# Performance work log

Measured on AMD Instinct MI355X. Metric: run time of the kernel, lower is better.

## Reference

```python
import jax, jax.numpy as jnp
import numpy as np

DIM_MODEL = 512
INV_SCALE = DIM_MODEL ** (-0.5)  # NOTE: source DIVIDES by this, i.e. multiplies scores by sqrt(d)


def setup_inputs() -> dict:
    key = jax.random.key(0)
    ks = jax.random.split(key, 9)
    B, LQ, LKV, D = 32, 64, 4096, DIM_MODEL
    lim = 1.0 / np.sqrt(D)  # torch Linear default init range
    return {
        "x1": jax.random.normal(ks[0], (B, LQ, D), dtype=jnp.float32),
        "x2": jax.random.normal(ks[1], (B, LKV, D), dtype=jnp.float32),
        "mask": jnp.zeros((B, LQ, LKV), dtype=bool),
        "wq": jax.random.uniform(ks[2], (D, D), jnp.float32, -lim, lim),
        "bq": jax.random.uniform(ks[3], (D,), jnp.float32, -lim, lim),
        "wk": jax.random.uniform(ks[4], (D, D), jnp.float32, -lim, lim),
        "bk": jax.random.uniform(ks[5], (D,), jnp.float32, -lim, lim),
        "wv": jax.random.uniform(ks[6], (D, D), jnp.float32, -lim, lim),
        "bv": jax.random.uniform(ks[7], (D,), jnp.float32, -lim, lim),
    }


def reference(x1, x2, mask, wq, bq, wk, bk, wv, bv):
    # torch.nn.Linear: y = x @ W^T + b
    q = jnp.einsum("bqd,ed->bqe", x1, wq) + bq          # [B, LQ, D]
    k = jnp.einsum("bkd,ed->bke", x2, wk) + bk          # [B, LKV, D]
    v = jnp.einsum("bkd,ed->bke", x2, wv) + bv          # [B, LKV, D]
    qk = jnp.einsum("bqd,bkd->bqk", q, k)               # [B, LQ, LKV]
    scaled_qk = qk / INV_SCALE                           # faithful: divide by d^-0.5
    p = jax.nn.softmax(scaled_qk, axis=-1)
    # dropout p=0.0 -> identity; mask is unused in the original forward
    return jnp.einsum("bqk,bkd->bqd", p, v)              # [B, LQ, D]
```

## Files before the change

### kernel.cpp

```cpp
#include <hip/hip_runtime.h>
#include <math.h>


#define LQ 64
#define LKV 4096
#define NB 32
#define DM 512
#define SCALE 22.627416997969522f
#define KEYS_TOTAL (NB * LKV)
#define NCHUNK 16
#define CHUNK 256
#define PBS 264

typedef __attribute__((ext_vector_type(8))) short bf16x8;
typedef __attribute__((ext_vector_type(4))) float f32x4;
typedef __attribute__((ext_vector_type(8))) unsigned short u16x8;
typedef __attribute__((ext_vector_type(4))) unsigned short u16x4;

__device__ __forceinline__ unsigned short f2bf(float f) {
    unsigned u = __float_as_uint(f);
    u += 0x7fffu + ((u >> 16) & 1u);
    return (unsigned short)(u >> 16);
}
__device__ __forceinline__ float bf2f(unsigned short s) {
    return __uint_as_float(((unsigned)s) << 16);
}
__device__ __forceinline__ void gld16(const void* g, void* l) {
    __builtin_amdgcn_global_load_lds(
        (const __attribute__((address_space(1))) unsigned int*)g,
        (__attribute__((address_space(3))) unsigned int*)l, 16, 0, 0);
}

__global__ __launch_bounds__(256) void split_kernel(const float* __restrict__ src,
                                                    unsigned short* __restrict__ hi,
                                                    unsigned short* __restrict__ lo) {
    size_t idx = ((size_t)blockIdx.x * 256 + threadIdx.x) * 8;
    float4 a = *(const float4*)(src + idx);
    float4 b = *(const float4*)(src + idx + 4);
    float ff[8] = {a.x, a.y, a.z, a.w, b.x, b.y, b.z, b.w};
    u16x8 h, l;
#pragma unroll
    for (int i = 0; i < 8; ++i) {
        h[i] = f2bf(ff[i]);
        l[i] = f2bf(ff[i] - bf2f(h[i]));
    }
    *(u16x8*)(hi + idx) = h;
    *(u16x8*)(lo + idx) = l;
}

__global__ __launch_bounds__(256) void transposeSplit_kernel(const float* __restrict__ in,
        unsigned short* __restrict__ hi, unsigned short* __restrict__ lo) {
    __shared__ float T[64 * 65];
    const int bx = blockIdx.x * 64, by = blockIdx.y * 64;
    const int t = threadIdx.x, col = t & 63, rg = t >> 6;
#pragma unroll
    for (int i = 0; i < 16; ++i) {
        int row = i * 4 + rg;
        T[col * 65 + row] = in[(size_t)(by + row) * DM + bx + col];
    }
    __syncthreads();
#pragma unroll
    for (int i = 0; i < 16; ++i) {
        int row = i * 4 + rg;
        float v = T[row * 65 + col];
        unsigned short h = f2bf(v);
        hi[(size_t)(bx + row) * DM + by + col] = h;
        lo[(size_t)(bx + row) * DM + by + col] = f2bf(v - bf2f(h));
    }
}

__global__ __launch_bounds__(256) void sgemm_kernel(
        const unsigned short* __restrict__ Ah_g, const unsigned short* __restrict__ Al_g,
        const unsigned short* __restrict__ Bh_g, const unsigned short* __restrict__ Bl_g,
        const float* __restrict__ bias, int mode,
        unsigned short* __restrict__ out0, unsigned short* __restrict__ out2l,
        float* __restrict__ outf) {
    __shared__ unsigned short smem[16384];
    unsigned short* Ah = smem;
    unsigned short* Al = smem + 4096;
    unsigned short* Bh = smem + 8192;
    unsigned short* Bl = smem + 12288;

    const int bn = blockIdx.x, bm = blockIdx.y;
    const int t = threadIdx.x, w = t >> 6, l = t & 63;
    const int wm = (w >> 1) * 64, wn = (w & 1) * 64;
    const int c16 = l & 15, q = l >> 4, q8 = q << 3;
    const int rB = l >> 2, cB = (l & 3) << 3;

    f32x4 acc[4][4];
#pragma unroll
    for (int i = 0; i < 4; ++i)
#pragma unroll
        for (int jj = 0; jj < 4; ++jj) acc[i][jj] = (f32x4){0.f,0.f,0.f,0.f};

    for (int k0 = 0; k0 < DM; k0 += 32) {
#pragma unroll
        for (int jj = 0; jj < 2; ++jj) {
            int r = w * 32 + jj * 16;
            size_t ga = (size_t)(bm * 128 + r + rB) * DM + k0 + cB;
            gld16(Ah_g + ga, &Ah[r * 32]);
            gld16(Al_g + ga, &Al[r * 32]);
            size_t gb = (size_t)(bn * 128 + r + rB) * DM + k0 + cB;
            gld16(Bh_g + gb, &Bh[r * 32]);
            gld16(Bl_g + gb, &Bl[r * 32]);
        }
        __syncthreads();
        bf16x8 ah[4], al[4];
#pragma unroll
        for (int mt = 0; mt < 4; ++mt) {
            ah[mt] = *(const bf16x8*)&Ah[(wm + mt*16 + c16) * 32 + q8];
            al[mt] = *(const bf16x8*)&Al[(wm + mt*16 + c16) * 32 + q8];
        }
#pragma unroll
        for (int nt = 0; nt < 4; ++nt) {
            bf16x8 bh = *(const bf16x8*)&Bh[(wn + nt*16 + c16) * 32 + q8];
            bf16x8 bl = *(const bf16x8*)&Bl[(wn + nt*16 + c16) * 32 + q8];
#pragma unroll
            for (int mt = 0; mt < 4; ++mt) {
                acc[mt][nt] = __builtin_amdgcn_mfma_f32_16x16x32_bf16(ah[mt], bh, acc[mt][nt], 0, 0, 0);
                acc[mt][nt] = __builtin_amdgcn_mfma_f32_16x16x32_bf16(al[mt], bh, acc[mt][nt], 0, 0, 0);
                acc[mt][nt] = __builtin_amdgcn_mfma_f32_16x16x32_bf16(ah[mt], bl, acc[mt][nt], 0, 0, 0);
            }
        }
        __syncthreads();
    }

#pragma unroll
    for (int mt = 0; mt < 4; ++mt)
#pragma unroll
        for (int nt = 0; nt < 4; ++nt) {
            int col = bn * 128 + wn + nt * 16 + c16;
            float bia = bias ? bias[col] : 0.f;
#pragma unroll
            for (int r = 0; r < 4; ++r) {
                size_t row = (size_t)bm * 128 + wm + mt * 16 + q * 4 + r;
                float y = acc[mt][nt][r] + bia;
                if (mode == 0) {
                    unsigned short h = f2bf(y);
                    out0[row * 1024 + col]       = h;
                    out0[row * 1024 + 512 + col] = f2bf(y - bf2f(h));
                } else if (mode == 1) {
                    outf[row * 512 + col] = y;
                } else {
                    unsigned short h = f2bf(y);
                    out0[row * 512 + col]  = h;
                    out2l[row * 512 + col] = f2bf(y - bf2f(h));
                }
            }
        }
}

__global__ __launch_bounds__(256) void splitT_kernel(const float* __restrict__ src,
        unsigned short* __restrict__ x2m, unsigned short* __restrict__ x2ht) {
    __shared__ unsigned short T[128 * 136];
    const int d0 = blockIdx.x * 128, k0 = blockIdx.y * 128;
    const int t = threadIdx.x;
    const int cg = t & 31, rg = t >> 5;
#pragma unroll
    for (int i = 0; i < 16; ++i) {
        int row = i * 8 + rg;
        float4 v = *(const float4*)(src + (size_t)(k0 + row) * DM + d0 + cg * 4);
        float ff[4] = {v.x, v.y, v.z, v.w};
        u16x4 h, lo_;
#pragma unroll
        for (int j = 0; j < 4; ++j) {
            h[j]   = f2bf(ff[j]);
            lo_[j] = f2bf(ff[j] - bf2f(h[j]));
        }
        size_t gm = (size_t)(k0 + row) * 1024 + d0 + cg * 4;
        *(u16x4*)(x2m + gm)       = h;
        *(u16x4*)(x2m + gm + 512) = lo_;
        int rsw = row ^ ((cg & 15) << 3);
#pragma unroll
        for (int j = 0; j < 4; ++j)
            T[(cg * 4 + j) * 136 + rsw] = h[j];
    }
    __syncthreads();
#pragma unroll
    for (int ii = 0; ii < 8; ++ii) {
        int dl = ii * 16 + (t >> 4);
        int ko = (t & 15) * 8;
        u16x8 vv = *(const u16x8*)&T[dl * 136 + (ko ^ (((dl >> 2) & 15) << 3))];
        *(u16x8*)(x2ht + (size_t)(d0 + dl) * KEYS_TOTAL + k0 + ko) = vv;
    }
}

__global__ __launch_bounds__(512, 4) void attn_kernel(
        const unsigned short* __restrict__ Q2,
        const unsigned short* __restrict__ K2,
        const unsigned short* __restrict__ Vt,
        float* __restrict__ Opart,
        float* __restrict__ ML) {
    __shared__ char smem_raw[81920];
    unsigned short* Pb = (unsigned short*)smem_raw;
    float* redb = (float*)(smem_raw + 66560);
    float* mrow = (float*)(smem_raw + 68608);
    float* lrow = (float*)(smem_raw + 68864);

    const int c = blockIdx.x, b = blockIdx.y;
    const int t = threadIdx.x, w = t >> 6, l = t & 63;
    const int c16 = l & 15, q = l >> 4, q8 = q << 3;
    const int rB = l >> 2, cB = (l & 3) << 3;
    const size_t key0 = (size_t)b * LKV + (size_t)c * CHUNK;

    f32x4 acc[4][2];
#pragma unroll
    for (int i = 0; i < 4; ++i)
#pragma unroll
        for (int jj = 0; jj < 2; ++jj) acc[i][jj] = (f32x4){0.f,0.f,0.f,0.f};

    auto stageQK = [&](int s, int k0) {
        char* base = smem_raw + s * 40960;
        unsigned short* Qh = (unsigned short*)base;
        unsigned short* Ql = (unsigned short*)(base + 4096);
        unsigned short* Kh = (unsigned short*)(base + 8192);
        unsigned short* Kl = (unsigned short*)(base + 24576);
        if (w < 4)
            gld16(Q2 + (size_t)(b * 64 + w * 16 + rB) * 1024 + k0 + cB, &Qh[(w * 16) * 32]);
        else
            gld16(Q2 + (size_t)(b * 64 + (w - 4) * 16 + rB) * 1024 + 512 + k0 + cB, &Ql[((w - 4) * 16) * 32]);
#pragma unroll
        for (int jj = 0; jj < 2; ++jj) {
            int r = w * 32 + jj * 16;
            size_t krow = key0 + r + rB;
            gld16(K2 + krow * 1024 + k0 + cB,       &Kh[r * 32]);
            gld16(K2 + krow * 1024 + 512 + k0 + cB, &Kl[r * 32]);
        }
    };

    stageQK(0, 0);
    __syncthreads();
#pragma unroll 1
    for (int k0 = 0; k0 < DM; k0 += 32) {
        const int s = (k0 >> 5) & 1;
        if (k0 + 32 < DM) stageQK(s ^ 1, k0 + 32);
        const unsigned short* Qh = (const unsigned short*)(smem_raw + s * 40960);
        const unsigned short* Ql = Qh + 2048;
        const unsigned short* Kh = Qh + 4096;
        const unsigned short* Kl = Qh + 12288;
        bf16x8 ah[4], al[4];
#pragma unroll
        for (int mt = 0; mt < 4; ++mt) {
            ah[mt] = *(const bf16x8*)&Qh[(mt * 16 + c16) * 32 + q8];
            al[mt] = *(const bf16x8*)&Ql[(mt * 16 + c16) * 32 + q8];
        }
#pragma unroll
        for (int nt = 0; nt < 2; ++nt) {
            bf16x8 bh = *(const bf16x8*)&Kh[(w * 32 + nt * 16 + c16) * 32 + q8];
            bf16x8 bl = *(const bf16x8*)&Kl[(w * 32 + nt * 16 + c16) * 32 + q8];
#pragma unroll
            for (int mt = 0; mt < 4; ++mt) {
                acc[mt][nt] = __builtin_amdgcn_mfma_f32_16x16x32_bf16(ah[mt], bh, acc[mt][nt], 0, 0, 0);
                acc[mt][nt] = __builtin_amdgcn_mfma_f32_16x16x32_bf16(al[mt], bh, acc[mt][nt], 0, 0, 0);
                acc[mt][nt] = __builtin_amdgcn_mfma_f32_16x16x32_bf16(ah[mt], bl, acc[mt][nt], 0, 0, 0);
            }
        }
        __syncthreads();
    }

    auto stagePV = [&](int s, int h, int ks) {
        unsigned short* Vb = (unsigned short*)(smem_raw + 33792 + s * 16384);
#pragma unroll
        for (int jj = 0; jj < 2; ++jj) {
            int dloc = w * 32 + jj * 16;
            gld16(Vt + (size_t)(h * 256 + dloc + rB) * KEYS_TOTAL + key0 + ks * 32 + cB,
                  &Vb[dloc * 32]);
        }
    };
    stagePV(0, 0, 0);

#pragma unroll
    for (int mt = 0; mt < 4; ++mt)
#pragma unroll
        for (int nt = 0; nt < 2; ++nt)
#pragma unroll
            for (int r = 0; r < 4; ++r) acc[mt][nt][r] *= SCALE;

    float rmax_[4][4];
#pragma unroll
    for (int mt = 0; mt < 4; ++mt)
#pragma unroll
        for (int r = 0; r < 4; ++r)
            rmax_[mt][r] = fmaxf(acc[mt][0][r], acc[mt][1][r]);
#pragma unroll
    for (int off = 1; off < 16; off <<= 1)
#pragma unroll
        for (int mt = 0; mt < 4; ++mt)
#pragma unroll
            for (int r = 0; r < 4; ++r)
                rmax_[mt][r] = fmaxf(rmax_[mt][r], __shfl_xor(rmax_[mt][r], off));
    if (c16 == 0) {
#pragma unroll
        for (int mt = 0; mt < 4; ++mt)
#pragma unroll
            for (int r = 0; r < 4; ++r) redb[w * 64 + mt * 16 + q * 4 + r] = rmax_[mt][r];
    }
    __syncthreads();
    if (t < 64) {
        float m = redb[t];
#pragma unroll
        for (int ww = 1; ww < 8; ++ww) m = fmaxf(m, redb[ww * 64 + t]);
        mrow[t] = m;
    }
    __syncthreads();

    float rsum_[4][4];
#pragma unroll
    for (int mt = 0; mt < 4; ++mt)
#pragma unroll
        for (int r = 0; r < 4; ++r) {
            float m = mrow[mt * 16 + q * 4 + r];
            float s = 0.f;
#pragma unroll
            for (int nt = 0; nt < 2; ++nt) {
                float e = __expf(acc[mt][nt][r] - m);
                acc[mt][nt][r] = e;
                s += e;
            }
            rsum_[mt][r] = s;
        }
#pragma unroll
    for (int off = 1; off < 16; off <<= 1)
#pragma unroll
        for (int mt = 0; mt < 4; ++mt)
#pragma unroll
            for (int r = 0; r < 4; ++r) rsum_[mt][r] += __shfl_xor(rsum_[mt][r], off);
    if (c16 == 0) {
#pragma unroll
        for (int mt = 0; mt < 4; ++mt)
#pragma unroll
            for (int r = 0; r < 4; ++r) redb[w * 64 + mt * 16 + q * 4 + r] = rsum_[mt][r];
    }
    __syncthreads();
    if (t < 64) {
        float s = redb[t];
#pragma unroll
        for (int ww = 1; ww < 8; ++ww) s += redb[ww * 64 + t];
        lrow[t] = s;
    }
#pragma unroll
    for (int mt = 0; mt < 4; ++mt)
#pragma unroll
        for (int nt = 0; nt < 2; ++nt)
#pragma unroll
            for (int r = 0; r < 4; ++r)
                Pb[(mt * 16 + q * 4 + r) * PBS + w * 32 + nt * 16 + c16] = f2bf(acc[mt][nt][r]);
    __syncthreads();

    f32x4 accO[4][4];
#pragma unroll
    for (int i = 0; i < 4; ++i)
#pragma unroll
        for (int jj = 0; jj < 4; ++jj) accO[i][jj] = (f32x4){0.f,0.f,0.f,0.f};

#pragma unroll 1
    for (int ks = 0; ks < 8; ++ks) {
        const int s = ks & 1;
        if (ks < 7) stagePV(s ^ 1, 0, ks + 1);
        else        stagePV(s ^ 1, 1, 0);
        const unsigned short* Vb = (const unsigned short*)(smem_raw + 33792 + s * 16384);
        bf16x8 ap[4];
#pragma unroll
        for (int mt = 0; mt < 4; ++mt)
            ap[mt] = *(const bf16x8*)&Pb[(mt * 16 + c16) * PBS + ks * 32 + q8];
#pragma unroll
        for (int nt = 0; nt < 2; ++nt) {
            bf16x8 bvv = *(const bf16x8*)&Vb[(w * 32 + nt * 16 + c16) * 32 + q8];
#pragma unroll
            for (int mt = 0; mt < 4; ++mt)
                accO[mt][nt] = __builtin_amdgcn_mfma_f32_16x16x32_bf16(ap[mt], bvv, accO[mt][nt], 0, 0, 0);
        }
        __syncthreads();
    }
#pragma unroll 1
    for (int ks = 0; ks < 8; ++ks) {
        const int s = ks & 1;
        if (ks < 7) stagePV(s ^ 1, 1, ks + 1);
        const unsigned short* Vb = (const unsigned short*)(smem_raw + 33792 + s * 16384);
        bf16x8 ap[4];
#pragma unroll
        for (int mt = 0; mt < 4; ++mt)
            ap[mt] = *(const bf16x8*)&Pb[(mt * 16 + c16) * PBS + ks * 32 + q8];
#pragma unroll
        for (int nt = 0; nt < 2; ++nt) {
            bf16x8 bvv = *(const bf16x8*)&Vb[(w * 32 + nt * 16 + c16) * 32 + q8];
#pragma unroll
            for (int mt = 0; mt < 4; ++mt)
                accO[mt][2 + nt] = __builtin_amdgcn_mfma_f32_16x16x32_bf16(ap[mt], bvv, accO[mt][2 + nt], 0, 0, 0);
        }
        __syncthreads();
    }

    const size_t part = (size_t)b * NCHUNK + c;
#pragma unroll
    for (int mt = 0; mt < 4; ++mt)
#pragma unroll
        for (int h = 0; h < 2; ++h)
#pragma unroll
            for (int nt = 0; nt < 2; ++nt) {
                int col = h * 256 + w * 32 + nt * 16 + c16;
#pragma unroll
                for (int r = 0; r < 4; ++r)
                    Opart[(part * 64 + mt * 16 + q * 4 + r) * 512 + col] = accO[mt][h * 2 + nt][r];
            }
    if (t < 64) {
        ML[part * 128 + t]      = mrow[t];
        ML[part * 128 + 64 + t] = lrow[t];
    }
}

__global__ __launch_bounds__(128) void combine_kernel(const float* __restrict__ Opart,
                                                      const float* __restrict__ ML,
                                                      unsigned short* __restrict__ Uh,
                                                      unsigned short* __restrict__ Ul) {
    const int b = blockIdx.x >> 6, row = blockIdx.x & 63;
    const int t = threadIdx.x;
    float m[NCHUNK], lv[NCHUNK];
    float M = -1e30f;
#pragma unroll
    for (int c = 0; c < NCHUNK; ++c) {
        m[c]  = ML[(size_t)(b * NCHUNK + c) * 128 + row];
        lv[c] = ML[(size_t)(b * NCHUNK + c) * 128 + 64 + row];
        M = fmaxf(M, m[c]);
    }
    float den = 0.f, wgt[NCHUNK];
#pragma unroll
    for (int c = 0; c < NCHUNK; ++c) { wgt[c] = __expf(m[c] - M); den += wgt[c] * lv[c]; }
    float4 o = make_float4(0.f, 0.f, 0.f, 0.f);
#pragma unroll
    for (int c = 0; c < NCHUNK; ++c) {
        float4 v = *(const float4*)&Opart[((size_t)(b * NCHUNK + c) * 64 + row) * 512 + t * 4];
        o.x += wgt[c] * v.x; o.y += wgt[c] * v.y; o.z += wgt[c] * v.z; o.w += wgt[c] * v.w;
    }
    const float inv = 1.f / den;
    float rr[4] = {o.x * inv, o.y * inv, o.z * inv, o.w * inv};
    u16x4 h, lo_;
#pragma unroll
    for (int j = 0; j < 4; ++j) {
        h[j]   = f2bf(rr[j]);
        lo_[j] = f2bf(rr[j] - bf2f(h[j]));
    }
    size_t base = ((size_t)(b * 64 + row)) * 512 + t * 4;
    *(u16x4*)&Uh[base] = h;
    *(u16x4*)&Ul[base] = lo_;
}

extern "C" void kernel_launch(void* const* d_in, const int* in_sizes, int n_in,
                              void* d_out, int out_size, void* d_ws, size_t ws_size,
                              hipStream_t stream) {
    const float* x1 = (const float*)d_in[0];
    const float* x2 = (const float*)d_in[1];
    const float* wq = (const float*)d_in[3];
    const float* bq = (const float*)d_in[4];
    const float* wk = (const float*)d_in[5];
    const float* wv = (const float*)d_in[7];
    const float* bv = (const float*)d_in[8];
    float* out = (float*)d_out;

    char* ws = (char*)d_ws;
    unsigned short* x2m   = (unsigned short*)(ws);
    unsigned short* x2ht  = (unsigned short*)(ws + 268435456);
    float*          Opart = (float*)(ws + 402653184);
    float*          ML    = (float*)(ws + 469762048);
    unsigned short* M2    = (unsigned short*)(ws + 470024192);
    unsigned short* x1h   = (unsigned short*)(ws + 474218496);
    unsigned short* x1l   = (unsigned short*)(ws + 476315648);
    unsigned short* Uh    = (unsigned short*)(ws + 478412800);
    unsigned short* Ul    = (unsigned short*)(ws + 480509952);
    unsigned short* q1h   = (unsigned short*)(ws + 482607104);
    unsigned short* q1l   = (unsigned short*)(ws + 484704256);
    unsigned short* wqh   = (unsigned short*)(ws + 486801408);
    unsigned short* wql   = (unsigned short*)(ws + 487325696);
    unsigned short* wkth  = (unsigned short*)(ws + 487849984);
    unsigned short* wktl  = (unsigned short*)(ws + 488374272);
    unsigned short* wvh   = (unsigned short*)(ws + 488898560);
    unsigned short* wvl   = (unsigned short*)(ws + 489422848);

    splitT_kernel<<<dim3(4, 1024), 256, 0, stream>>>(x2, x2m, x2ht);

    split_kernel<<<512, 256, 0, stream>>>(x1, x1h, x1l);
    split_kernel<<<128, 256, 0, stream>>>(wq, wqh, wql);
    transposeSplit_kernel<<<dim3(8, 8), 256, 0, stream>>>(wk, wkth, wktl);
    split_kernel<<<128, 256, 0, stream>>>(wv, wvh, wvl);
    sgemm_kernel<<<dim3(4, 16), 256, 0, stream>>>(x1h, x1l, wqh, wql,
                                                  bq, 2, q1h, q1l, nullptr);
    sgemm_kernel<<<dim3(4, 16), 256, 0, stream>>>(q1h, q1l, wkth, wktl,
                                                  nullptr, 0, M2, nullptr, nullptr);

    attn_kernel<<<dim3(NCHUNK, NB), 512, 0, stream>>>(M2, x2m, x2ht, Opart, ML);
    combine_kernel<<<NB * LQ, 128, 0, stream>>>(Opart, ML, Uh, Ul);

    sgemm_kernel<<<dim3(4, 16), 256, 0, stream>>>(Uh, Ul, wvh, wvl,
                                                  bv, 1, nullptr, nullptr, out);
}
```

Before: 663.3 us.

## Split x2 into bf16 hi/lo inside attention kernel instead of materializing

The attention kernel now loads fp32 x2 rows straight into shared memory and does the bf16 hi/lo split in registers before the MFMAs. This drops the x2m intermediate buffer (write plus re-read of 256MB). The Vt transpose kernel no longer writes x2m. The four small weight and x1 split launches are merged into one prep kernel to cut launch overhead. In exchange the attention inner loop gains conversion ALU work and LDS reads of fp32 data.

```diff
diff --git a/kernel.cpp b/kernel.cpp
--- a/kernel.cpp
+++ b/kernel.cpp
@@ -31,10 +31,10 @@
         (__attribute__((address_space(3))) unsigned int*)l, 16, 0, 0);
 }
 
-__global__ __launch_bounds__(256) void split_kernel(const float* __restrict__ src,
-                                                    unsigned short* __restrict__ hi,
-                                                    unsigned short* __restrict__ lo) {
-    size_t idx = ((size_t)blockIdx.x * 256 + threadIdx.x) * 8;
+__device__ __forceinline__ void split8_body(const float* __restrict__ src,
+                                            unsigned short* __restrict__ hi,
+                                            unsigned short* __restrict__ lo, int blk) {
+    size_t idx = ((size_t)blk * 256 + threadIdx.x) * 8;
     float4 a = *(const float4*)(src + idx);
     float4 b = *(const float4*)(src + idx + 4);
     float ff[8] = {a.x, a.y, a.z, a.w, b.x, b.y, b.z, b.w};
@@ -48,25 +48,40 @@
     *(u16x8*)(lo + idx) = l;
 }
 
-__global__ __launch_bounds__(256) void transposeSplit_kernel(const float* __restrict__ in,
-        unsigned short* __restrict__ hi, unsigned short* __restrict__ lo) {
+__global__ __launch_bounds__(256) void prep_kernel(
+        const float* __restrict__ x1, const float* __restrict__ wq,
+        const float* __restrict__ wk, const float* __restrict__ wv,
+        unsigned short* __restrict__ x1h, unsigned short* __restrict__ x1l,
+        unsigned short* __restrict__ wqh, unsigned short* __restrict__ wql,
+        unsigned short* __restrict__ wkth, unsigned short* __restrict__ wktl,
+        unsigned short* __restrict__ wvh, unsigned short* __restrict__ wvl) {
     __shared__ float T[64 * 65];
-    const int bx = blockIdx.x * 64, by = blockIdx.y * 64;
-    const int t = threadIdx.x, col = t & 63, rg = t >> 6;
-#pragma unroll
-    for (int i = 0; i < 16; ++i) {
-        int row = i * 4 + rg;
-        T[col * 65 + row] = in[(size_t)(by + row) * DM + bx + col];
-    }
-    __syncthreads();
-#pragma unroll
-    for (int i = 0; i < 16; ++i) {
-        int row = i * 4 + rg;
-        float v = T[row * 65 + col];
-        unsigned short h = f2bf(v);
-        hi[(size_t)(bx + row) * DM + by + col] = h;
-        lo[(size_t)(bx + row) * DM + by + col] = f2bf(v - bf2f(h));
-    }
+    int bid = blockIdx.x;
+    if (bid < 512) { split8_body(x1, x1h, x1l, bid); return; }
+    bid -= 512;
+    if (bid < 128) { split8_body(wq, wqh, wql, bid); return; }
+    bid -= 128;
+    if (bid < 64) {
+        const int bx = (bid & 7) * 64, by = (bid >> 3) * 64;
+        const int t = threadIdx.x, col = t & 63, rg = t >> 6;
+#pragma unroll
+        for (int i = 0; i < 16; ++i) {
+            int row = i * 4 + rg;
+            T[col * 65 + row] = wk[(size_t)(by + row) * DM + bx + col];
+        }
+        __syncthreads();
+#pragma unroll
+        for (int i = 0; i < 16; ++i) {
+            int row = i * 4 + rg;
+            float v = T[row * 65 + col];
+            unsigned short h = f2bf(v);
+            wkth[(size_t)(bx + row) * DM + by + col] = h;
+            wktl[(size_t)(bx + row) * DM + by + col] = f2bf(v - bf2f(h));
+        }
+        return;
+    }
+    bid -= 64;
+    split8_body(wv, wvh, wvl, bid);
 }
 
 __global__ __launch_bounds__(256) void sgemm_kernel(
@@ -150,8 +165,8 @@
         }
 }
 
-__global__ __launch_bounds__(256) void splitT_kernel(const float* __restrict__ src,
-        unsigned short* __restrict__ x2m, unsigned short* __restrict__ x2ht) {
+__global__ __launch_bounds__(256) void prepVt_kernel(const float* __restrict__ src,
+        unsigned short* __restrict__ x2ht) {
     __shared__ unsigned short T[128 * 136];
     const int d0 = blockIdx.x * 128, k0 = blockIdx.y * 128;
     const int t = threadIdx.x;
@@ -161,19 +176,10 @@
         int row = i * 8 + rg;
         float4 v = *(const float4*)(src + (size_t)(k0 + row) * DM + d0 + cg * 4);
         float ff[4] = {v.x, v.y, v.z, v.w};
-        u16x4 h, lo_;
-#pragma unroll
-        for (int j = 0; j < 4; ++j) {
-            h[j]   = f2bf(ff[j]);
-            lo_[j] = f2bf(ff[j] - bf2f(h[j]));
-        }
-        size_t gm = (size_t)(k0 + row) * 1024 + d0 + cg * 4;
-        *(u16x4*)(x2m + gm)       = h;
-        *(u16x4*)(x2m + gm + 512) = lo_;
         int rsw = row ^ ((cg & 15) << 3);
 #pragma unroll
         for (int j = 0; j < 4; ++j)
-            T[(cg * 4 + j) * 136 + rsw] = h[j];
+            T[(cg * 4 + j) * 136 + rsw] = f2bf(ff[j]);
     }
     __syncthreads();
 #pragma unroll
@@ -187,7 +193,7 @@
 
 __global__ __launch_bounds__(512, 4) void attn_kernel(
         const unsigned short* __restrict__ Q2,
-        const unsigned short* __restrict__ K2,
+        const float* __restrict__ x2f,
         const unsigned short* __restrict__ Vt,
         float* __restrict__ Opart,
         float* __restrict__ ML) {
@@ -201,6 +207,7 @@
     const int t = threadIdx.x, w = t >> 6, l = t & 63;
     const int c16 = l & 15, q = l >> 4, q8 = q << 3;
     const int rB = l >> 2, cB = (l & 3) << 3;
+    const int rF = l >> 3, cF = (l & 7) << 2;
     const size_t key0 = (size_t)b * LKV + (size_t)c * CHUNK;
 
     f32x4 acc[4][2];
@@ -213,18 +220,15 @@
         char* base = smem_raw + s * 40960;
         unsigned short* Qh = (unsigned short*)base;
         unsigned short* Ql = (unsigned short*)(base + 4096);
-        unsigned short* Kh = (unsigned short*)(base + 8192);
-        unsigned short* Kl = (unsigned short*)(base + 24576);
+        float* Kf = (float*)(base + 8192);
         if (w < 4)
             gld16(Q2 + (size_t)(b * 64 + w * 16 + rB) * 1024 + k0 + cB, &Qh[(w * 16) * 32]);
         else
             gld16(Q2 + (size_t)(b * 64 + (w - 4) * 16 + rB) * 1024 + 512 + k0 + cB, &Ql[((w - 4) * 16) * 32]);
 #pragma unroll
-        for (int jj = 0; jj < 2; ++jj) {
-            int r = w * 32 + jj * 16;
-            size_t krow = key0 + r + rB;
-            gld16(K2 + krow * 1024 + k0 + cB,       &Kh[r * 32]);
-            gld16(K2 + krow * 1024 + 512 + k0 + cB, &Kl[r * 32]);
+        for (int i = 0; i < 4; ++i) {
+            int r = w * 32 + i * 8;
+            gld16(x2f + (key0 + r + rF) * DM + k0 + cF, &Kf[r * 32]);
         }
     };
 
@@ -236,8 +240,7 @@
         if (k0 + 32 < DM) stageQK(s ^ 1, k0 + 32);
         const unsigned short* Qh = (const unsigned short*)(smem_raw + s * 40960);
         const unsigned short* Ql = Qh + 2048;
-        const unsigned short* Kh = Qh + 4096;
-        const unsigned short* Kl = Qh + 12288;
+        const float* Kf = (const float*)(smem_raw + s * 40960 + 8192);
         bf16x8 ah[4], al[4];
 #pragma unroll
         for (int mt = 0; mt < 4; ++mt) {
@@ -246,8 +249,17 @@
         }
 #pragma unroll
         for (int nt = 0; nt < 2; ++nt) {
-            bf16x8 bh = *(const bf16x8*)&Kh[(w * 32 + nt * 16 + c16) * 32 + q8];
-            bf16x8 bl = *(const bf16x8*)&Kl[(w * 32 + nt * 16 + c16) * 32 + q8];
+            const float* kp = &Kf[(w * 32 + nt * 16 + c16) * 32 + q8];
+            float4 f0 = *(const float4*)kp;
+            float4 f1 = *(const float4*)(kp + 4);
+            float ff[8] = {f0.x, f0.y, f0.z, f0.w, f1.x, f1.y, f1.z, f1.w};
+            bf16x8 bh, bl;
+#pragma unroll
+            for (int i2 = 0; i2 < 8; ++i2) {
+                unsigned short hb = f2bf(ff[i2]);
+                bh[i2] = (short)hb;
+                bl[i2] = (short)f2bf(ff[i2] - bf2f(hb));
+            }
 #pragma unroll
             for (int mt = 0; mt < 4; ++mt) {
                 acc[mt][nt] = __builtin_amdgcn_mfma_f32_16x16x32_bf16(ah[mt], bh, acc[mt][nt], 0, 0, 0);
@@ -458,36 +470,35 @@
     float* out = (float*)d_out;
 
     char* ws = (char*)d_ws;
-    unsigned short* x2m   = (unsigned short*)(ws);
-    unsigned short* x2ht  = (unsigned short*)(ws + 268435456);
-    float*          Opart = (float*)(ws + 402653184);
-    float*          ML    = (float*)(ws + 469762048);
-    unsigned short* M2    = (unsigned short*)(ws + 470024192);
-    unsigned short* x1h   = (unsigned short*)(ws + 474218496);
-    unsigned short* x1l   = (unsigned short*)(ws + 476315648);
-    unsigned short* Uh    = (unsigned short*)(ws + 478412800);
-    unsigned short* Ul    = (unsigned short*)(ws + 480509952);
-    unsigned short* q1h   = (unsigned short*)(ws + 482607104);
-    unsigned short* q1l   = (unsigned short*)(ws + 484704256);
-    unsigned short* wqh   = (unsigned short*)(ws + 486801408);
-    unsigned short* wql   = (unsigned short*)(ws + 487325696);
-    unsigned short* wkth  = (unsigned short*)(ws + 487849984);
-    unsigned short* wktl  = (unsigned short*)(ws + 488374272);
-    unsigned short* wvh   = (unsigned short*)(ws + 488898560);
-    unsigned short* wvl   = (unsigned short*)(ws + 489422848);
-
-    splitT_kernel<<<dim3(4, 1024), 256, 0, stream>>>(x2, x2m, x2ht);
-
-    split_kernel<<<512, 256, 0, stream>>>(x1, x1h, x1l);
-    split_kernel<<<128, 256, 0, stream>>>(wq, wqh, wql);
-    transposeSplit_kernel<<<dim3(8, 8), 256, 0, stream>>>(wk, wkth, wktl);
-    split_kernel<<<128, 256, 0, stream>>>(wv, wvh, wvl);
+    unsigned short* x2ht  = (unsigned short*)(ws);
+    float*          Opart = (float*)(ws + 134217728);
+    float*          ML    = (float*)(ws + 201326592);
+    unsigned short* M2    = (unsigned short*)(ws + 201588736);
+    unsigned short* x1h   = (unsigned short*)(ws + 205783040);
+    unsigned short* x1l   = (unsigned short*)(ws + 207880192);
+    unsigned short* Uh    = (unsigned short*)(ws + 209977344);
+    unsigned short* Ul    = (unsigned short*)(ws + 212074496);
+    unsigned short* q1h   = (unsigned short*)(ws + 214171648);
+    unsigned short* q1l   = (unsigned short*)(ws + 216268800);
+    unsigned short* wqh   = (unsigned short*)(ws + 218365952);
+    unsigned short* wql   = (unsigned short*)(ws + 218890240);
+    unsigned short* wkth  = (unsigned short*)(ws + 219414528);
+    unsigned short* wktl  = (unsigned short*)(ws + 219938816);
+    unsigned short* wvh   = (unsigned short*)(ws + 220463104);
+    unsigned short* wvl   = (unsigned short*)(ws + 220987392);
+
+    prepVt_kernel<<<dim3(4, 1024), 256, 0, stream>>>(x2, x2ht);
+
+    prep_kernel<<<832, 256, 0, stream>>>(x1, wq, wk, wv,
+                                         x1h, x1l, wqh, wql,
+                                         wkth, wktl, wvh, wvl);
+
     sgemm_kernel<<<dim3(4, 16), 256, 0, stream>>>(x1h, x1l, wqh, wql,
                                                   bq, 2, q1h, q1l, nullptr);
     sgemm_kernel<<<dim3(4, 16), 256, 0, stream>>>(q1h, q1l, wkth, wktl,
                                                   nullptr, 0, M2, nullptr, nullptr);
 
-    attn_kernel<<<dim3(NCHUNK, NB), 512, 0, stream>>>(M2, x2m, x2ht, Opart, ML);
+    attn_kernel<<<dim3(NCHUNK, NB), 512, 0, stream>>>(M2, x2, x2ht, Opart, ML);
     combine_kernel<<<NB * LQ, 128, 0, stream>>>(Opart, ML, Uh, Ul);
 
     sgemm_kernel<<<dim3(4, 16), 256, 0, stream>>>(Uh, Ul, wvh, wvl,
```

Result: faster. 596.3 us (-10.1%).
